# Optimization experiments

Measured on AMD Instinct MI355X. Metric: run time of the kernel, lower is better.

The kernel has to match this reference:

```python
import jax, jax.numpy as jnp
import numpy as np

IN_FEATS = 768   # xlm-roberta-base hidden size
HIDDEN = 128     # hardcoded in GCNEncoder
OUT_FEATS = 128
NUM_GRAPHS = 1024
NODES_PER_GRAPH = 256
N = NUM_GRAPHS * NODES_PER_GRAPH
N_CLASS = 2


def setup_inputs() -> dict:
    key = jax.random.key(0)
    ks = jax.random.split(key, 12)
    s = lambda fan_in: 1.0 / np.sqrt(fan_in)
    return {
        "x": jax.random.normal(ks[0], (N, IN_FEATS), dtype=jnp.float32),
        "prompt_node": jax.random.normal(ks[1], (IN_FEATS,), dtype=jnp.float32),
        "class_nodes": jax.random.normal(ks[2], (N_CLASS, IN_FEATS), dtype=jnp.float32),
        "W1": jax.random.uniform(ks[3], (IN_FEATS, HIDDEN), jnp.float32, -s(IN_FEATS), s(IN_FEATS)),
        "b1": jnp.zeros((HIDDEN,), jnp.float32),
        "W2": jax.random.uniform(ks[4], (HIDDEN, OUT_FEATS), jnp.float32, -s(HIDDEN), s(HIDDEN)),
        "b2": jnp.zeros((OUT_FEATS,), jnp.float32),
        "Wfc": jax.random.uniform(ks[5], (OUT_FEATS, N_CLASS), jnp.float32, -s(OUT_FEATS), s(OUT_FEATS)),
        "bfc": jnp.zeros((N_CLASS,), jnp.float32),
        "num_graphs": NUM_GRAPHS,
    }


def _gcn_conv(h_in, W, b, src, dst, num_nodes):
    # PyG GCNConv: add self loops, symmetric norm D^-1/2 (A+I) D^-1/2, then X W + b.
    deg = jax.ops.segment_sum(jnp.ones_like(src, dtype=h_in.dtype), dst,
                              num_segments=num_nodes) + 1.0  # +1 for self loop
    dinv = deg ** -0.5
    h = h_in @ W                                    # [num_nodes, out]
    norm = dinv[src] * dinv[dst]                    # [E]
    agg = jax.ops.segment_sum(h[src] * norm[:, None], dst, num_segments=num_nodes)
    agg = agg + (dinv * dinv)[:, None] * h          # self-loop contribution
    return agg + b


def reference(x, prompt_node, class_nodes, W1, b1, W2, b2, Wfc, bfc, num_graphs):
    G = int(num_graphs)
    N_orig = x.shape[0]
    n_per = N_orig // G
    n_cls = class_nodes.shape[0]
    total = N_orig + G + G * n_cls

    # construct_prompted_graph: append prompt nodes then class nodes (tiled per graph)
    full_x = jnp.concatenate([
        x,
        jnp.broadcast_to(prompt_node, (G, prompt_node.shape[0])),
        jnp.tile(class_nodes, (G, 1)),
    ], axis=0)

    # star edges: node -> prompt, prompt -> class; then to_undirected (both dirs)
    src1 = jnp.arange(N_orig)
    dst1 = N_orig + jnp.repeat(jnp.arange(G), n_per)
    src2 = jnp.repeat(N_orig + jnp.arange(G), n_cls)
    dst2 = N_orig + G + jnp.arange(G * n_cls)
    src = jnp.concatenate([src1, src2, dst1, dst2])
    dst = jnp.concatenate([dst1, dst2, src1, src2])

    h = _gcn_conv(full_x, W1, b1, src, dst, total)
    h = jax.nn.relu(h)  # dropout omitted (eval mode)
    h = _gcn_conv(h, W2, b2, src, dst, total)

    class_idx = N_orig + G + jnp.arange(G * n_cls)
    class_emb = h[class_idx]                         # [G*n_cls, OUT_FEATS]
    logits = class_emb @ Wfc + bfc                   # [G*n_cls, 2]
    return jax.nn.log_softmax(logits, axis=-1)
```

## Files before the change

kernel.cpp:

```cpp
#include <hip/hip_runtime.h>
#include <math.h>

namespace {
constexpr int IN_FEATS = 768;
constexpr int HIDDEN   = 128;
constexpr int G        = 1024;
constexpr int NPG      = 256;
constexpr int C4       = IN_FEATS / 4;
constexpr int NT       = 384;
constexpr int GPB      = 2;
constexpr int NB       = G / GPB;
typedef float f32x4 __attribute__((ext_vector_type(4)));
}

__global__ __launch_bounds__(NT) void fused_kernel(
    const float* __restrict__ x, const float* __restrict__ prompt,
    const float* __restrict__ cls,
    const float* __restrict__ W1, const float* __restrict__ b1,
    const float* __restrict__ W2, const float* __restrict__ b2,
    const float* __restrict__ Wfc, const float* __restrict__ bfc,
    float* __restrict__ out)
{
    __shared__ __align__(16) float S[GPB][IN_FEATS];
    __shared__ f32x4  partA[GPB][2][C4];
    __shared__ float  pb[3][5][HIDDEN];
    __shared__ __align__(16) float rbuf[4][HIDDEN];
    __shared__ float  red[2][2];

    const int g0  = blockIdx.x * GPB;
    const int tid = threadIdx.x;
    const float ainv = 1.0f / sqrtf(518.0f);

    const int p  = tid / C4;
    const int c4 = tid % C4;
    const f32x4* xb  = reinterpret_cast<const f32x4*>(x);
    const f32x4* xp0 = xb + ((size_t)(g0 + 0) * NPG + p) * C4 + c4;
    const f32x4* xp1 = xb + ((size_t)(g0 + 1) * NPG + p) * C4 + c4;
    {
        f32x4 a0 = (f32x4)0.0f, a1 = a0, a2 = a0, a3 = a0;
        f32x4 b0 = a0, b1 = a0, b2 = a0, b3 = a0;
        for (int i = 0; i < NPG / 2; i += 4) {
            const f32x4 v0 = __builtin_nontemporal_load(xp0 + (size_t)(2 * (i + 0)) * C4);
            const f32x4 v1 = __builtin_nontemporal_load(xp0 + (size_t)(2 * (i + 1)) * C4);
            const f32x4 v2 = __builtin_nontemporal_load(xp0 + (size_t)(2 * (i + 2)) * C4);
            const f32x4 v3 = __builtin_nontemporal_load(xp0 + (size_t)(2 * (i + 3)) * C4);
            const f32x4 w0 = __builtin_nontemporal_load(xp1 + (size_t)(2 * (i + 0)) * C4);
            const f32x4 w1 = __builtin_nontemporal_load(xp1 + (size_t)(2 * (i + 1)) * C4);
            const f32x4 w2 = __builtin_nontemporal_load(xp1 + (size_t)(2 * (i + 2)) * C4);
            const f32x4 w3 = __builtin_nontemporal_load(xp1 + (size_t)(2 * (i + 3)) * C4);
            a0 += v0; a1 += v1; a2 += v2; a3 += v3;
            b0 += w0; b1 += w1; b2 += w2; b3 += w3;
        }
        partA[0][p][c4] = (a0 + a1) + (a2 + a3);
        partA[1][p][c4] = (b0 + b1) + (b2 + b3);
    }
    __syncthreads();
    {
        const int gg = tid / C4;
        const int c  = tid % C4;
        const f32x4 q0 = partA[gg][0][c], q1 = partA[gg][1][c];
        *reinterpret_cast<f32x4*>(&S[gg][c * 4]) = q0 + q1;
    }
    __syncthreads();

    {
        const int seg = tid >> 7;
        const int j   = tid & (HIDDEN - 1);
        const int cb  = seg * 256;
        const float* w1p = W1 + (size_t)cb * HIDDEN + j;
        float t0 = 0.f, t1 = 0.f, hp = 0.f, h0 = 0.f, h1 = 0.f;
        for (int cc = 0; cc < 256; cc += 4) {
            const int c = cb + cc;
            const f32x4 s0 = *reinterpret_cast<const f32x4*>(&S[0][c]);
            const f32x4 s1 = *reinterpret_cast<const f32x4*>(&S[1][c]);
            const f32x4 pv = *reinterpret_cast<const f32x4*>(prompt + c);
            const f32x4 k0 = *reinterpret_cast<const f32x4*>(cls + c);
            const f32x4 k1 = *reinterpret_cast<const f32x4*>(cls + IN_FEATS + c);
            const float w0 = w1p[(size_t)(cc + 0) * HIDDEN];
            const float w1 = w1p[(size_t)(cc + 1) * HIDDEN];
            const float w2 = w1p[(size_t)(cc + 2) * HIDDEN];
            const float w3 = w1p[(size_t)(cc + 3) * HIDDEN];
            t0 = fmaf(s0.x, w0, t0); t1 = fmaf(s1.x, w0, t1);
            hp = fmaf(pv.x, w0, hp); h0 = fmaf(k0.x, w0, h0); h1 = fmaf(k1.x, w0, h1);
            t0 = fmaf(s0.y, w1, t0); t1 = fmaf(s1.y, w1, t1);
            hp = fmaf(pv.y, w1, hp); h0 = fmaf(k0.y, w1, h0); h1 = fmaf(k1.y, w1, h1);
            t0 = fmaf(s0.z, w2, t0); t1 = fmaf(s1.z, w2, t1);
            hp = fmaf(pv.z, w2, hp); h0 = fmaf(k0.z, w2, h0); h1 = fmaf(k1.z, w2, h1);
            t0 = fmaf(s0.w, w3, t0); t1 = fmaf(s1.w, w3, t1);
            hp = fmaf(pv.w, w3, hp); h0 = fmaf(k0.w, w3, h0); h1 = fmaf(k1.w, w3, h1);
        }
        pb[seg][0][j] = t0; pb[seg][1][j] = t1;
        pb[seg][2][j] = hp; pb[seg][3][j] = h0; pb[seg][4][j] = h1;
    }
    __syncthreads();
    if (tid < HIDDEN) {
        const float t0 = pb[0][0][tid] + pb[1][0][tid] + pb[2][0][tid];
        const float t1 = pb[0][1][tid] + pb[1][1][tid] + pb[2][1][tid];
        const float hp = pb[0][2][tid] + pb[1][2][tid] + pb[2][2][tid];
        const float h0 = pb[0][3][tid] + pb[1][3][tid] + pb[2][3][tid];
        const float h1 = pb[0][4][tid] + pb[1][4][tid] + pb[2][4][tid];
        const float b  = b1[tid];
        const float C1 = ainv * (h0 + h1) + hp * (1.0f / 259.0f) + b;
        rbuf[0][tid] = fmaxf(fmaf(ainv, t0, C1), 0.f);
        rbuf[1][tid] = fmaxf(fmaf(ainv, t1, C1), 0.f);
        rbuf[2][tid] = fmaxf(fmaf(ainv, hp, fmaf(0.5f, h0, b)), 0.f);
        rbuf[3][tid] = fmaxf(fmaf(ainv, hp, fmaf(0.5f, h1, b)), 0.f);
    }
    __syncthreads();

    float u0 = 0.f, u1 = 0.f, uc0 = 0.f, uc1 = 0.f;
    if (tid < HIDDEN) {
        const float* w2p = W2 + tid;
        for (int c = 0; c < HIDDEN; c += 4) {
            const f32x4 r0 = *reinterpret_cast<const f32x4*>(&rbuf[0][c]);
            const f32x4 r1 = *reinterpret_cast<const f32x4*>(&rbuf[1][c]);
            const f32x4 q0 = *reinterpret_cast<const f32x4*>(&rbuf[2][c]);
            const f32x4 q1 = *reinterpret_cast<const f32x4*>(&rbuf[3][c]);
            const float wa = w2p[(size_t)(c + 0) * HIDDEN];
            const float wb = w2p[(size_t)(c + 1) * HIDDEN];
            const float wc = w2p[(size_t)(c + 2) * HIDDEN];
            const float wd = w2p[(size_t)(c + 3) * HIDDEN];
            u0  = fmaf(r0.x, wa, u0);  u1  = fmaf(r1.x, wa, u1);
            uc0 = fmaf(q0.x, wa, uc0); uc1 = fmaf(q1.x, wa, uc1);
            u0  = fmaf(r0.y, wb, u0);  u1  = fmaf(r1.y, wb, u1);
            uc0 = fmaf(q0.y, wb, uc0); uc1 = fmaf(q1.y, wb, uc1);
            u0  = fmaf(r0.z, wc, u0);  u1  = fmaf(r1.z, wc, u1);
            uc0 = fmaf(q0.z, wc, uc0); uc1 = fmaf(q1.z, wc, uc1);
            u0  = fmaf(r0.w, wd, u0);  u1  = fmaf(r1.w, wd, u1);
            uc0 = fmaf(q0.w, wd, uc0); uc1 = fmaf(q1.w, wd, uc1);
        }
    }

    const float bfc0 = bfc[0], bfc1 = bfc[1];
    for (int gg = 0; gg < GPB; ++gg) {
        for (int k = 0; k < 2; ++k) {
            float p0 = 0.f, p1 = 0.f;
            if (tid < HIDDEN) {
                const float ug = (gg == 0) ? u0 : u1;
                const float uk = (k == 0) ? uc0 : uc1;
                const float v  = fmaf(ainv, ug, fmaf(0.5f, uk, b2[tid]));
                p0 = v * Wfc[tid * 2 + 0];
                p1 = v * Wfc[tid * 2 + 1];
                #pragma unroll
                for (int off = 32; off > 0; off >>= 1) {
                    p0 += __shfl_down(p0, off);
                    p1 += __shfl_down(p1, off);
                }
                if ((tid & 63) == 0) { red[tid >> 6][0] = p0; red[tid >> 6][1] = p1; }
            }
            __syncthreads();
            if (tid == 0) {
                const float l0 = red[0][0] + red[1][0] + bfc0;
                const float l1 = red[0][1] + red[1][1] + bfc1;
                const float m   = fmaxf(l0, l1);
                const float lse = m + logf(expf(l0 - m) + expf(l1 - m));
                float* o = out + ((size_t)(g0 + gg) * 2 + k) * 2;
                o[0] = l0 - lse;
                o[1] = l1 - lse;
            }
            __syncthreads();
        }
    }
}

extern "C" void kernel_launch(void* const* d_in, const int* in_sizes, int n_in,
                              void* d_out, int out_size, void* d_ws, size_t ws_size,
                              hipStream_t stream) {
    const float* x      = (const float*)d_in[0];
    const float* prompt = (const float*)d_in[1];
    const float* cls    = (const float*)d_in[2];
    const float* W1     = (const float*)d_in[3];
    const float* b1     = (const float*)d_in[4];
    const float* W2     = (const float*)d_in[5];
    const float* b2     = (const float*)d_in[6];
    const float* Wfc    = (const float*)d_in[7];
    const float* bfc    = (const float*)d_in[8];
    float* out = (float*)d_out;

    fused_kernel<<<NB, NT, 0, stream>>>(x, prompt, cls, W1, b1, W2, b2,
                                        Wfc, bfc, out);
}
```

Before: 160.0 us.

## Overlap second graph's feature streaming with first graph's W1 projection

Each block now reduces the node features of its first graph alone, then streams the second graph's rows inside the W1 matvec loop for the first graph, so the global loads overlap with the FMA work. The second graph's projection runs as a separate pass afterward. The goal is to hide memory latency behind compute in a bandwidth-bound kernel. In exchange, each block does fewer loads in flight during the first phase and needs an extra sync and a second pass over W1.

```diff
diff --git a/kernel.cpp b/kernel.cpp
--- a/kernel.cpp
+++ b/kernel.cpp
@@ -22,7 +22,7 @@
     float* __restrict__ out)
 {
     __shared__ __align__(16) float S[GPB][IN_FEATS];
-    __shared__ f32x4  partA[GPB][2][C4];
+    __shared__ f32x4  partA[2][C4];
     __shared__ float  pb[3][5][HIDDEN];
     __shared__ __align__(16) float rbuf[4][HIDDEN];
     __shared__ float  red[2][2];
@@ -36,30 +36,22 @@
     const f32x4* xb  = reinterpret_cast<const f32x4*>(x);
     const f32x4* xp0 = xb + ((size_t)(g0 + 0) * NPG + p) * C4 + c4;
     const f32x4* xp1 = xb + ((size_t)(g0 + 1) * NPG + p) * C4 + c4;
+
     {
         f32x4 a0 = (f32x4)0.0f, a1 = a0, a2 = a0, a3 = a0;
-        f32x4 b0 = a0, b1 = a0, b2 = a0, b3 = a0;
         for (int i = 0; i < NPG / 2; i += 4) {
             const f32x4 v0 = __builtin_nontemporal_load(xp0 + (size_t)(2 * (i + 0)) * C4);
             const f32x4 v1 = __builtin_nontemporal_load(xp0 + (size_t)(2 * (i + 1)) * C4);
             const f32x4 v2 = __builtin_nontemporal_load(xp0 + (size_t)(2 * (i + 2)) * C4);
             const f32x4 v3 = __builtin_nontemporal_load(xp0 + (size_t)(2 * (i + 3)) * C4);
-            const f32x4 w0 = __builtin_nontemporal_load(xp1 + (size_t)(2 * (i + 0)) * C4);
-            const f32x4 w1 = __builtin_nontemporal_load(xp1 + (size_t)(2 * (i + 1)) * C4);
-            const f32x4 w2 = __builtin_nontemporal_load(xp1 + (size_t)(2 * (i + 2)) * C4);
-            const f32x4 w3 = __builtin_nontemporal_load(xp1 + (size_t)(2 * (i + 3)) * C4);
             a0 += v0; a1 += v1; a2 += v2; a3 += v3;
-            b0 += w0; b1 += w1; b2 += w2; b3 += w3;
-        }
-        partA[0][p][c4] = (a0 + a1) + (a2 + a3);
-        partA[1][p][c4] = (b0 + b1) + (b2 + b3);
-    }
-    __syncthreads();
-    {
-        const int gg = tid / C4;
-        const int c  = tid % C4;
-        const f32x4 q0 = partA[gg][0][c], q1 = partA[gg][1][c];
-        *reinterpret_cast<f32x4*>(&S[gg][c * 4]) = q0 + q1;
+        }
+        partA[p][c4] = (a0 + a1) + (a2 + a3);
+    }
+    __syncthreads();
+    if (tid < C4) {
+        const f32x4 q0 = partA[0][tid], q1 = partA[1][tid];
+        *reinterpret_cast<f32x4*>(&S[0][tid * 4]) = q0 + q1;
     }
     __syncthreads();
 
@@ -68,37 +60,80 @@
         const int j   = tid & (HIDDEN - 1);
         const int cb  = seg * 256;
         const float* w1p = W1 + (size_t)cb * HIDDEN + j;
-        float t0 = 0.f, t1 = 0.f, hp = 0.f, h0 = 0.f, h1 = 0.f;
+        float t0 = 0.f, hp = 0.f, h0 = 0.f, h1 = 0.f;
+        f32x4 a0 = (f32x4)0.0f, a1 = a0, a2 = a0, a3 = a0;
+
+#define B0_COLS(CC)                                                          \
+        {                                                                    \
+            const int c = cb + (CC);                                         \
+            const f32x4 s0 = *reinterpret_cast<const f32x4*>(&S[0][c]);      \
+            const f32x4 pv = *reinterpret_cast<const f32x4*>(prompt + c);    \
+            const f32x4 k0 = *reinterpret_cast<const f32x4*>(cls + c);       \
+            const f32x4 k1 = *reinterpret_cast<const f32x4*>(cls + IN_FEATS + c); \
+            const float w0 = w1p[(size_t)((CC) + 0) * HIDDEN];               \
+            const float w1 = w1p[(size_t)((CC) + 1) * HIDDEN];               \
+            const float w2 = w1p[(size_t)((CC) + 2) * HIDDEN];               \
+            const float w3 = w1p[(size_t)((CC) + 3) * HIDDEN];               \
+            t0 = fmaf(s0.x, w0, t0); hp = fmaf(pv.x, w0, hp);                \
+            h0 = fmaf(k0.x, w0, h0); h1 = fmaf(k1.x, w0, h1);                \
+            t0 = fmaf(s0.y, w1, t0); hp = fmaf(pv.y, w1, hp);                \
+            h0 = fmaf(k0.y, w1, h0); h1 = fmaf(k1.y, w1, h1);                \
+            t0 = fmaf(s0.z, w2, t0); hp = fmaf(pv.z, w2, hp);                \
+            h0 = fmaf(k0.z, w2, h0); h1 = fmaf(k1.z, w2, h1);                \
+            t0 = fmaf(s0.w, w3, t0); hp = fmaf(pv.w, w3, hp);                \
+            h0 = fmaf(k0.w, w3, h0); h1 = fmaf(k1.w, w3, h1);                \
+        }
+
+        for (int cc = 0; cc < 256; cc += 8) {
+            const int l = cc >> 1;
+            const f32x4 xv0 = __builtin_nontemporal_load(xp1 + (size_t)(2 * (l + 0)) * C4);
+            const f32x4 xv1 = __builtin_nontemporal_load(xp1 + (size_t)(2 * (l + 1)) * C4);
+            B0_COLS(cc);
+            a0 += xv0; a1 += xv1;
+            const f32x4 xv2 = __builtin_nontemporal_load(xp1 + (size_t)(2 * (l + 2)) * C4);
+            const f32x4 xv3 = __builtin_nontemporal_load(xp1 + (size_t)(2 * (l + 3)) * C4);
+            B0_COLS(cc + 4);
+            a2 += xv2; a3 += xv3;
+        }
+#undef B0_COLS
+        pb[seg][0][j] = t0; pb[seg][1][j] = hp;
+        pb[seg][2][j] = h0; pb[seg][3][j] = h1;
+        partA[p][c4] = (a0 + a1) + (a2 + a3);
+    }
+    __syncthreads();
+    if (tid < C4) {
+        const f32x4 q0 = partA[0][tid], q1 = partA[1][tid];
+        *reinterpret_cast<f32x4*>(&S[1][tid * 4]) = q0 + q1;
+    }
+    __syncthreads();
+
+    {
+        const int seg = tid >> 7;
+        const int j   = tid & (HIDDEN - 1);
+        const int cb  = seg * 256;
+        const float* w1p = W1 + (size_t)cb * HIDDEN + j;
+        float t1 = 0.f;
         for (int cc = 0; cc < 256; cc += 4) {
             const int c = cb + cc;
-            const f32x4 s0 = *reinterpret_cast<const f32x4*>(&S[0][c]);
             const f32x4 s1 = *reinterpret_cast<const f32x4*>(&S[1][c]);
-            const f32x4 pv = *reinterpret_cast<const f32x4*>(prompt + c);
-            const f32x4 k0 = *reinterpret_cast<const f32x4*>(cls + c);
-            const f32x4 k1 = *reinterpret_cast<const f32x4*>(cls + IN_FEATS + c);
             const float w0 = w1p[(size_t)(cc + 0) * HIDDEN];
             const float w1 = w1p[(size_t)(cc + 1) * HIDDEN];
             const float w2 = w1p[(size_t)(cc + 2) * HIDDEN];
             const float w3 = w1p[(size_t)(cc + 3) * HIDDEN];
-            t0 = fmaf(s0.x, w0, t0); t1 = fmaf(s1.x, w0, t1);
-            hp = fmaf(pv.x, w0, hp); h0 = fmaf(k0.x, w0, h0); h1 = fmaf(k1.x, w0, h1);
-            t0 = fmaf(s0.y, w1, t0); t1 = fmaf(s1.y, w1, t1);
-            hp = fmaf(pv.y, w1, hp); h0 = fmaf(k0.y, w1, h0); h1 = fmaf(k1.y, w1, h1);
-            t0 = fmaf(s0.z, w2, t0); t1 = fmaf(s1.z, w2, t1);
-            hp = fmaf(pv.z, w2, hp); h0 = fmaf(k0.z, w2, h0); h1 = fmaf(k1.z, w2, h1);
-            t0 = fmaf(s0.w, w3, t0); t1 = fmaf(s1.w, w3, t1);
-            hp = fmaf(pv.w, w3, hp); h0 = fmaf(k0.w, w3, h0); h1 = fmaf(k1.w, w3, h1);
-        }
-        pb[seg][0][j] = t0; pb[seg][1][j] = t1;
-        pb[seg][2][j] = hp; pb[seg][3][j] = h0; pb[seg][4][j] = h1;
+            t1 = fmaf(s1.x, w0, t1);
+            t1 = fmaf(s1.y, w1, t1);
+            t1 = fmaf(s1.z, w2, t1);
+            t1 = fmaf(s1.w, w3, t1);
+        }
+        pb[seg][4][j] = t1;
     }
     __syncthreads();
     if (tid < HIDDEN) {
         const float t0 = pb[0][0][tid] + pb[1][0][tid] + pb[2][0][tid];
-        const float t1 = pb[0][1][tid] + pb[1][1][tid] + pb[2][1][tid];
-        const float hp = pb[0][2][tid] + pb[1][2][tid] + pb[2][2][tid];
-        const float h0 = pb[0][3][tid] + pb[1][3][tid] + pb[2][3][tid];
-        const float h1 = pb[0][4][tid] + pb[1][4][tid] + pb[2][4][tid];
+        const float hp = pb[0][1][tid] + pb[1][1][tid] + pb[2][1][tid];
+        const float h0 = pb[0][2][tid] + pb[1][2][tid] + pb[2][2][tid];
+        const float h1 = pb[0][3][tid] + pb[1][3][tid] + pb[2][3][tid];
+        const float t1 = pb[0][4][tid] + pb[1][4][tid] + pb[2][4][tid];
         const float b  = b1[tid];
         const float C1 = ainv * (h0 + h1) + hp * (1.0f / 259.0f) + b;
         rbuf[0][tid] = fmaxf(fmaf(ainv, t0, C1), 0.f);
```

Result: faster. 154.1 us (-3.6%).
